# Optimization experiments

Measured on AMD Instinct MI355X. Metric: run time of the kernel, lower is better.

## Reference

```python
import jax, jax.numpy as jnp
import numpy as np

N, C, H, W = 16, 256, 64, 64
KC, VC, HEADS = 256, 256, 8

def setup_inputs() -> dict:
    key = jax.random.key(0)
    ks = jax.random.split(key, 9)
    s = 0.02
    return {
        "x": jax.random.normal(ks[0], (N, C, H, W), dtype=jnp.float32),
        "Wk": jax.random.normal(ks[1], (KC, C), dtype=jnp.float32) * s,
        "bk": jax.random.normal(ks[2], (KC,), dtype=jnp.float32) * s,
        "Wq": jax.random.normal(ks[3], (KC, C), dtype=jnp.float32) * s,
        "bq": jax.random.normal(ks[4], (KC,), dtype=jnp.float32) * s,
        "Wv": jax.random.normal(ks[5], (VC, C), dtype=jnp.float32) * s,
        "bv": jax.random.normal(ks[6], (VC,), dtype=jnp.float32) * s,
        "Wr": jax.random.normal(ks[7], (C, VC), dtype=jnp.float32) * s,
        "br": jax.random.normal(ks[8], (C,), dtype=jnp.float32) * s,
    }

def reference(x, Wk, bk, Wq, bq, Wv, bv, Wr, br):
    n, c, h, w = x.shape
    hw = h * w
    hk = KC // HEADS   # per-head key channels
    hv = VC // HEADS   # per-head value channels
    # 1x1 convs as channel matmuls
    keys = jnp.einsum('oi,nihw->nohw', Wk, x) + bk[None, :, None, None]
    queries = jnp.einsum('oi,nihw->nohw', Wq, x) + bq[None, :, None, None]
    values = jnp.einsum('oi,nihw->nohw', Wv, x) + bv[None, :, None, None]
    # split heads: (n, heads, ch_per_head, hw)
    k = keys.reshape(n, HEADS, hk, hw)
    q = queries.reshape(n, HEADS, hk, hw)
    v = values.reshape(n, HEADS, hv, hw)
    k = jax.nn.softmax(k, axis=3)   # softmax over spatial positions
    q = jax.nn.softmax(q, axis=2)   # softmax over key channels
    # context: (n, heads, hk, hv)
    ctx = jnp.einsum('nhkl,nhvl->nhkv', k, v)
    # attended: (n, heads, hv, hw)
    att = jnp.einsum('nhkv,nhkl->nhvl', ctx, q)
    agg = att.reshape(n, VC, h, w)
    out = jnp.einsum('ov,nvhw->nohw', Wr, agg) + br[None, :, None, None] + x
    return out
```

## Files before the change

### kernel.cpp

```cpp
#include <hip/hip_runtime.h>

#define NB   16
#define CD   256
#define HWD  4096

typedef __attribute__((ext_vector_type(8))) short short8;
typedef __attribute__((ext_vector_type(4))) float f32x4;

static __device__ __forceinline__ float b2f(unsigned short u) {
  union { unsigned int i; float f; } x; x.i = ((unsigned int)u) << 16; return x.f;
}
static __device__ __forceinline__ unsigned short f2b(float f) {
  union { float f; unsigned int i; } x; x.f = f;
  return (unsigned short)((x.i + 0x7fffu + ((x.i >> 16) & 1u)) >> 16);
}

static __device__ __forceinline__ void gload16(const void* g, const unsigned short* l) {
  __builtin_amdgcn_global_load_lds(
      (const __attribute__((address_space(1))) void*)g,
      (__attribute__((address_space(3))) void*)l, 16, 0, 0);
}

__global__ __launch_bounds__(256)
void prep_kernel(const float* __restrict__ Wk, const float* __restrict__ Wq,
                 const float* __restrict__ Wv, unsigned short* __restrict__ Wc)
{
  int e4 = blockIdx.x * 256 + threadIdx.x;
  int base = e4 * 4;
  int w = base >> 16, off = base & 65535;
  const float* W = (w == 0) ? Wk : (w == 1) ? Wq : Wv;
  f32x4 v = *(const f32x4*)(W + off);
  unsigned int lo = (unsigned int)f2b(v.x) | ((unsigned int)f2b(v.y) << 16);
  unsigned int hi = (unsigned int)f2b(v.z) | ((unsigned int)f2b(v.w) << 16);
  *(uint2*)(Wc + base) = make_uint2(lo, hi);
}

__global__ __launch_bounds__(256)
void xt_kernel(const float* __restrict__ x, unsigned short* __restrict__ xT)
{
  __shared__ __align__(16) unsigned short T[64 * 80];
  const int t = threadIdx.x;
  const int l0 = blockIdx.x * 64, c0 = blockIdx.y * 64, n = blockIdx.z;
  const float* xn = x + (size_t)n * CD * HWD;
#pragma unroll
  for (int i = 0; i < 4; ++i) {
    int idx = t + i * 256;
    int c = idx >> 4, l4 = (idx & 15) * 4;
    f32x4 v = *(const f32x4*)(xn + (size_t)(c0 + c) * HWD + l0 + l4);
    T[(l4 + 0) * 80 + c] = f2b(v.x);
    T[(l4 + 1) * 80 + c] = f2b(v.y);
    T[(l4 + 2) * 80 + c] = f2b(v.z);
    T[(l4 + 3) * 80 + c] = f2b(v.w);
  }
  __syncthreads();
  unsigned short* dst = xT + ((size_t)n * HWD + l0) * CD + c0;
#pragma unroll
  for (int i = 0; i < 2; ++i) {
    int e = t + i * 256;
    int lr = e >> 3, c8 = (e & 7) * 8;
    *(short8*)(dst + (size_t)lr * CD + c8) = *(const short8*)(T + lr * 80 + c8);
  }
}

__global__ __launch_bounds__(256, 4)
void kqv_kernel(const unsigned short* __restrict__ Wc,
                const unsigned short* __restrict__ xT,
                const float* __restrict__ bk, const float* __restrict__ bq,
                const float* __restrict__ bv,
                unsigned short* __restrict__ keys,
                unsigned short* __restrict__ qsmT,
                unsigned short* __restrict__ vals)
{
  __shared__ __align__(16) unsigned short smem[17408];

  const int t  = threadIdx.x;
  const int lt = blockIdx.x;
  const int mt = blockIdx.y;
  const int n  = blockIdx.z;
  const int l0 = lt * 128;
  const int m0 = mt * 128;
  const int wsel = m0 >> 8;
  const int ocbase = m0 & 255;

  const unsigned short* Ag  = Wc;
  const unsigned short* Btn = xT + (size_t)n * HWD * CD;

  const int w = t >> 6, lane = t & 63;
  const int wr = (w >> 1) * 64, wc = (w & 1) * 64;
  const int lhi = lane >> 4, llo = lane & 15;

  f32x4 acc[4][4] = {};

  auto stage = [&](int buf, int ks) {
    unsigned short* As = smem + buf * 8192;
    unsigned short* Bs = As + 4096;
    const int k0 = ks * 32;
#pragma unroll
    for (int i = 0; i < 2; ++i) {
      int s   = t + i * 256;
      int row = s >> 2;
      int src = (((s ^ row) & 3)) << 3;
      gload16(Ag  + (size_t)(m0 + row) * CD + k0 + src, As + s * 8);
      gload16(Btn + (size_t)(l0 + row) * CD + k0 + src, Bs + s * 8);
    }
  };

  auto compute = [&](int buf) {
    const unsigned short* As = smem + buf * 8192;
    const unsigned short* Bs = As + 4096;
    const int slot = (lhi ^ (llo & 3)) * 8;
    short8 a[4], b[4];
#pragma unroll
    for (int mi = 0; mi < 4; ++mi)
      a[mi] = *(const short8*)(As + (wr + mi * 16 + llo) * 32 + slot);
#pragma unroll
    for (int ni = 0; ni < 4; ++ni)
      b[ni] = *(const short8*)(Bs + (wc + ni * 16 + llo) * 32 + slot);
#pragma unroll
    for (int mi = 0; mi < 4; ++mi)
#pragma unroll
      for (int ni = 0; ni < 4; ++ni)
        acc[mi][ni] = __builtin_amdgcn_mfma_f32_16x16x32_bf16(a[mi], b[ni], acc[mi][ni], 0, 0, 0);
  };

  stage(0, 0);
  __syncthreads();
#pragma unroll
  for (int ks = 0; ks < 8; ++ks) {
    if (ks < 7) stage((ks + 1) & 1, ks + 1);
    compute(ks & 1);
    __syncthreads();
  }

  const float* bias = (wsel == 0) ? bk : (wsel == 1) ? bq : bv;
#pragma unroll
  for (int mi = 0; mi < 4; ++mi) {
#pragma unroll
    for (int r = 0; r < 4; ++r) {
      float bb = bias[ocbase + wr + mi * 16 + lhi * 4 + r];
#pragma unroll
      for (int ni = 0; ni < 4; ++ni) acc[mi][ni][r] += bb;
    }
  }

  if (wsel == 1) {
#pragma unroll
    for (int g = 0; g < 2; ++g) {
#pragma unroll
      for (int ni = 0; ni < 4; ++ni) {
        float m = -1e30f;
#pragma unroll
        for (int mi = 2 * g; mi < 2 * g + 2; ++mi)
#pragma unroll
          for (int r = 0; r < 4; ++r) m = fmaxf(m, acc[mi][ni][r]);
        m = fmaxf(m, __shfl_xor(m, 16));
        m = fmaxf(m, __shfl_xor(m, 32));
        float s = 0.f;
#pragma unroll
        for (int mi = 2 * g; mi < 2 * g + 2; ++mi)
#pragma unroll
          for (int r = 0; r < 4; ++r) {
            float e = __expf(acc[mi][ni][r] - m);
            acc[mi][ni][r] = e;
            s += e;
          }
        s += __shfl_xor(s, 16);
        s += __shfl_xor(s, 32);
        float inv = 1.f / s;
#pragma unroll
        for (int mi = 2 * g; mi < 2 * g + 2; ++mi)
#pragma unroll
          for (int r = 0; r < 4; ++r) acc[mi][ni][r] *= inv;
      }
    }
    unsigned short* Co2 = smem;
#pragma unroll
    for (int mi = 0; mi < 4; ++mi)
#pragma unroll
      for (int ni = 0; ni < 4; ++ni) {
        int col = wc + ni * 16 + llo;
#pragma unroll
        for (int r = 0; r < 4; ++r) {
          int row = wr + mi * 16 + lhi * 4 + r;
          Co2[col * 136 + row] = f2b(acc[mi][ni][r]);
        }
      }
    __syncthreads();
    unsigned short* dst = qsmT + ((size_t)n * HWD + l0) * CD + ocbase;
#pragma unroll
    for (int i = 0; i < 8; ++i) {
      int e = t + i * 256;
      int l = e >> 4, c8 = (e & 15) * 8;
      *(short8*)(dst + (size_t)l * CD + c8) = *(const short8*)(Co2 + l * 136 + c8);
    }
  } else {
    unsigned short* Co = smem;
#pragma unroll
    for (int mi = 0; mi < 4; ++mi)
#pragma unroll
      for (int ni = 0; ni < 4; ++ni) {
        int col = wc + ni * 16 + llo;
#pragma unroll
        for (int r = 0; r < 4; ++r) {
          int row = wr + mi * 16 + lhi * 4 + r;
          Co[row * 136 + col] = f2b(acc[mi][ni][r]);
        }
      }
    __syncthreads();
    unsigned short* dst = ((wsel == 0) ? keys : vals)
                          + ((size_t)(n * CD + (wsel == 0 ? ocbase : ocbase))) * HWD + l0;
#pragma unroll
    for (int i = 0; i < 8; ++i) {
      int e = t + i * 256;
      int row = e >> 4, c8 = (e & 15) * 8;
      *(short8*)(dst + (size_t)row * HWD + c8) = *(const short8*)(Co + row * 136 + c8);
    }
  }
}

__global__ __launch_bounds__(256)
void rowstats_kernel(const unsigned short* __restrict__ keys,
                     float* __restrict__ stats)
{
  __shared__ float red[8];
  const int r = blockIdx.x;
  const int t = threadIdx.x;
  const unsigned short* rowp = keys + (size_t)r * HWD;
  float v[16];
  float m = -1e30f;
#pragma unroll
  for (int i = 0; i < 2; ++i) {
    const short8 u = *(const short8*)(rowp + t * 8 + i * 2048);
#pragma unroll
    for (int j = 0; j < 8; ++j) {
      v[i * 8 + j] = b2f((unsigned short)u[j]);
      m = fmaxf(m, v[i * 8 + j]);
    }
  }
#pragma unroll
  for (int off = 1; off < 64; off <<= 1) m = fmaxf(m, __shfl_xor(m, off));
  if ((t & 63) == 0) red[t >> 6] = m;
  __syncthreads();
  m = fmaxf(fmaxf(red[0], red[1]), fmaxf(red[2], red[3]));
  float s = 0.f;
#pragma unroll
  for (int i = 0; i < 16; ++i) s += __expf(v[i] - m);
#pragma unroll
  for (int off = 1; off < 64; off <<= 1) s += __shfl_xor(s, off);
  if ((t & 63) == 0) red[4 + (t >> 6)] = s;
  __syncthreads();
  if (t == 0) {
    s = red[4] + red[5] + red[6] + red[7];
    stats[r * 2]     = m;
    stats[r * 2 + 1] = 1.f / s;
  }
}

__global__ __launch_bounds__(256)
void ctx_kernel(const unsigned short* __restrict__ keys,
                const unsigned short* __restrict__ vals,
                const float* __restrict__ stats,
                float* __restrict__ ctxp)
{
  __shared__ float Cs[4][32][33];
  const int hf = blockIdx.x;
  const int nh = blockIdx.y;
  const int n = nh >> 3, h = nh & 7;
  const int t = threadIdx.x, w = t >> 6, lane = t & 63;
  const int lhi = lane >> 4, llo = lane & 15;
  const int lbase = hf * 2048 + w * 512;

  const unsigned short* kr = keys + (size_t)(n * CD + h * 32) * HWD;
  const unsigned short* vr = vals + (size_t)(n * CD + h * 32) * HWD;

  float mx[2], inv[2];
#pragma unroll
  for (int mi = 0; mi < 2; ++mi) {
    int kc = mi * 16 + llo;
    mx[mi]  = stats[(n * CD + h * 32 + kc) * 2];
    inv[mi] = stats[(n * CD + h * 32 + kc) * 2 + 1];
  }

  f32x4 acc[2][2] = {};
  for (int ks = 0; ks < 16; ++ks) {
    const int loff = lbase + ks * 32 + lhi * 8;
    short8 a[2], b[2];
#pragma unroll
    for (int mi = 0; mi < 2; ++mi) {
      const short8 u = *(const short8*)(kr + (size_t)(mi * 16 + llo) * HWD + loff);
      short8 af;
#pragma unroll
      for (int j = 0; j < 8; ++j)
        af[j] = (short)f2b(__expf(b2f((unsigned short)u[j]) - mx[mi]) * inv[mi]);
      a[mi] = af;
    }
#pragma unroll
    for (int ni = 0; ni < 2; ++ni)
      b[ni] = *(const short8*)(vr + (size_t)(ni * 16 + llo) * HWD + loff);
    acc[0][0] = __builtin_amdgcn_mfma_f32_16x16x32_bf16(a[0], b[0], acc[0][0], 0, 0, 0);
    acc[0][1] = __builtin_amdgcn_mfma_f32_16x16x32_bf16(a[0], b[1], acc[0][1], 0, 0, 0);
    acc[1][0] = __builtin_amdgcn_mfma_f32_16x16x32_bf16(a[1], b[0], acc[1][0], 0, 0, 0);
    acc[1][1] = __builtin_amdgcn_mfma_f32_16x16x32_bf16(a[1], b[1], acc[1][1], 0, 0, 0);
  }

#pragma unroll
  for (int mi = 0; mi < 2; ++mi)
#pragma unroll
    for (int ni = 0; ni < 2; ++ni)
#pragma unroll
      for (int r = 0; r < 4; ++r)
        Cs[w][mi * 16 + lhi * 4 + r][ni * 16 + llo] = acc[mi][ni][r];
  __syncthreads();
#pragma unroll
  for (int i = 0; i < 4; ++i) {
    int e = t + i * 256;
    int kc = e >> 5, vc = e & 31;
    float sum = Cs[0][kc][vc] + Cs[1][kc][vc] + Cs[2][kc][vc] + Cs[3][kc][vc];
    ctxp[((size_t)hf * 128 + nh) * 1024 + e] = sum;
  }
}

__global__ __launch_bounds__(256)
void proj_kernel(const float* __restrict__ ctxp, const float* __restrict__ Wr,
                 unsigned short* __restrict__ M)
{
  __shared__ float cs[32][33];
  const int nh = blockIdx.x;
  const int n = nh >> 3, h = nh & 7;
  const int t = threadIdx.x;
#pragma unroll
  for (int i = 0; i < 4; ++i) {
    int e = t + i * 256;
    cs[e >> 5][e & 31] = ctxp[(size_t)nh * 1024 + e] + ctxp[((size_t)128 + nh) * 1024 + e];
  }
  __syncthreads();
  float wreg[32];
  const float* wp = Wr + (size_t)t * 256 + h * 32;
#pragma unroll
  for (int i = 0; i < 8; ++i) {
    f32x4 v = *(const f32x4*)(wp + i * 4);
    wreg[i * 4] = v.x; wreg[i * 4 + 1] = v.y; wreg[i * 4 + 2] = v.z; wreg[i * 4 + 3] = v.w;
  }
  unsigned short o16[32];
#pragma unroll
  for (int kc = 0; kc < 32; ++kc) {
    float s = 0.f;
#pragma unroll
    for (int vv = 0; vv < 32; ++vv) s += wreg[vv] * cs[kc][vv];
    o16[kc] = f2b(s);
  }
  unsigned short* mp = M + (size_t)(n * CD + t) * 256 + h * 32;
#pragma unroll
  for (int i = 0; i < 8; ++i) {
    unsigned int lo = (unsigned int)o16[i * 4]     | ((unsigned int)o16[i * 4 + 1] << 16);
    unsigned int hi = (unsigned int)o16[i * 4 + 2] | ((unsigned int)o16[i * 4 + 3] << 16);
    *(uint2*)(mp + i * 4) = make_uint2(lo, hi);
  }
}

__global__ __launch_bounds__(256, 4)
void out_kernel(const unsigned short* __restrict__ M,
                const unsigned short* __restrict__ qsmT,
                const float* __restrict__ br,
                const float* __restrict__ x,
                float* __restrict__ out)
{
  __shared__ __align__(16) unsigned short smem[16384];

  const int t = threadIdx.x;
  const int lt = blockIdx.x;
  const int mt = blockIdx.y;
  const int n  = blockIdx.z;
  const int l0 = lt * 128, m0 = mt * 128;

  const unsigned short* Ag  = M + (size_t)n * CD * 256;
  const unsigned short* Btn = qsmT + (size_t)n * HWD * CD;

  const int w = t >> 6, lane = t & 63;
  const int wr = (w >> 1) * 64, wc = (w & 1) * 64;
  const int lhi = lane >> 4, llo = lane & 15;

  f32x4 acc[4][4] = {};

  auto stage = [&](int buf, int ks) {
    unsigned short* As = smem + buf * 8192;
    unsigned short* Bs = As + 4096;
    const int k0 = ks * 32;
#pragma unroll
    for (int i = 0; i < 2; ++i) {
      int s   = t + i * 256;
      int row = s >> 2;
      int src = (((s ^ row) & 3)) << 3;
      gload16(Ag  + (size_t)(m0 + row) * CD + k0 + src, As + s * 8);
      gload16(Btn + (size_t)(l0 + row) * CD + k0 + src, Bs + s * 8);
    }
  };

  auto compute = [&](int buf) {
    const unsigned short* As = smem + buf * 8192;
    const unsigned short* Bs = As + 4096;
    const int slot = (lhi ^ (llo & 3)) * 8;
    short8 a[4], b[4];
#pragma unroll
    for (int mi = 0; mi < 4; ++mi)
      a[mi] = *(const short8*)(As + (wr + mi * 16 + llo) * 32 + slot);
#pragma unroll
    for (int ni = 0; ni < 4; ++ni)
      b[ni] = *(const short8*)(Bs + (wc + ni * 16 + llo) * 32 + slot);
#pragma unroll
    for (int mi = 0; mi < 4; ++mi)
#pragma unroll
      for (int ni = 0; ni < 4; ++ni)
        acc[mi][ni] = __builtin_amdgcn_mfma_f32_16x16x32_bf16(a[mi], b[ni], acc[mi][ni], 0, 0, 0);
  };

  stage(0, 0);
  __syncthreads();
#pragma unroll
  for (int ks = 0; ks < 8; ++ks) {
    if (ks < 7) stage((ks + 1) & 1, ks + 1);
    compute(ks & 1);
    __syncthreads();
  }

  const float* xn = x + (size_t)n * CD * HWD;
  float* on = out + (size_t)n * CD * HWD;
#pragma unroll
  for (int mi = 0; mi < 4; ++mi)
#pragma unroll
    for (int r = 0; r < 4; ++r) {
      int row = m0 + wr + mi * 16 + lhi * 4 + r;
      float bb = br[row];
#pragma unroll
      for (int ni = 0; ni < 4; ++ni) {
        int col = l0 + wc + ni * 16 + llo;
        size_t off = (size_t)row * HWD + col;
        on[off] = acc[mi][ni][r] + bb + xn[off];
      }
    }
}

extern "C" void kernel_launch(void* const* d_in, const int* in_sizes, int n_in,
                              void* d_out, int out_size, void* d_ws, size_t ws_size,
                              hipStream_t stream) {
  const float* x  = (const float*)d_in[0];
  const float* Wk = (const float*)d_in[1];
  const float* bk = (const float*)d_in[2];
  const float* Wq = (const float*)d_in[3];
  const float* bq = (const float*)d_in[4];
  const float* Wv = (const float*)d_in[5];
  const float* bv = (const float*)d_in[6];
  const float* Wr = (const float*)d_in[7];
  const float* br = (const float*)d_in[8];
  float* out = (float*)d_out;

  char* ws = (char*)d_ws;
  unsigned short* keys = (unsigned short*)(ws);
  unsigned short* vals = (unsigned short*)(ws + 33554432);
  unsigned short* qsmT = (unsigned short*)(ws + 67108864);
  float* stats         = (float*)(ws + 100663296);
  float* ctxp          = (float*)(ws + 100696064);
  unsigned short* M    = (unsigned short*)(ws + 101744640);
  unsigned short* Wc   = (unsigned short*)(ws + 103841792);
  unsigned short* xT   = (unsigned short*)d_out;

  hipLaunchKernelGGL(prep_kernel, dim3(192), dim3(256), 0, stream, Wk, Wq, Wv, Wc);
  hipLaunchKernelGGL(xt_kernel, dim3(64, 4, NB), dim3(256), 0, stream, x, xT);
  hipLaunchKernelGGL(kqv_kernel, dim3(32, 6, NB), dim3(256), 0, stream,
                     Wc, xT, bk, bq, bv, keys, qsmT, vals);
  hipLaunchKernelGGL(rowstats_kernel, dim3(NB * CD), dim3(256), 0, stream, keys, stats);
  hipLaunchKernelGGL(ctx_kernel, dim3(2, 128), dim3(256), 0, stream,
                     keys, vals, stats, ctxp);
  hipLaunchKernelGGL(proj_kernel, dim3(128), dim3(256), 0, stream, ctxp, Wr, M);
  hipLaunchKernelGGL(out_kernel, dim3(32, 2, NB), dim3(256), 0, stream,
                     M, qsmT, br, x, out);
}
```

Measured before the change: 144.2 us.

## Use 64x64 output tiles with full-K single-shot LDS staging in out_kernel

The output GEMM kernel moves from 128x128 tiles with a double-buffered K loop of 32-wide stages to 64x64 tiles that load the entire K=256 slab of both operands into LDS at once, with a new XOR swizzle. The grid grows fourfold (64x4x16 blocks) and each wave computes a 2x2 MFMA block. The aim is more parallelism and fewer barriers in the memory-bound epilogue that reads x and writes out. The cost is lower data reuse per tile, more redundant loads of M and qsmT, and 64KB of LDS per block, which reduces occupancy (launch bounds drop to 2).

```diff
diff --git a/kernel.cpp b/kernel.cpp
--- a/kernel.cpp
+++ b/kernel.cpp
@@ -208,7 +208,7 @@
       }
     __syncthreads();
     unsigned short* dst = ((wsel == 0) ? keys : vals)
-                          + ((size_t)(n * CD + (wsel == 0 ? ocbase : ocbase))) * HWD + l0;
+                          + ((size_t)(n * CD + ocbase)) * HWD + l0;
 #pragma unroll
     for (int i = 0; i < 8; ++i) {
       int e = t + i * 256;
@@ -358,81 +358,74 @@
   }
 }
 
-__global__ __launch_bounds__(256, 4)
+__global__ __launch_bounds__(256, 2)
 void out_kernel(const unsigned short* __restrict__ M,
                 const unsigned short* __restrict__ qsmT,
                 const float* __restrict__ br,
                 const float* __restrict__ x,
                 float* __restrict__ out)
 {
-  __shared__ __align__(16) unsigned short smem[16384];
-
-  const int t = threadIdx.x;
+  __shared__ __align__(16) unsigned short smem[32768];
+  unsigned short* As = smem;
+  unsigned short* Bs = smem + 16384;
+
+  const int t  = threadIdx.x;
   const int lt = blockIdx.x;
   const int mt = blockIdx.y;
   const int n  = blockIdx.z;
-  const int l0 = lt * 128, m0 = mt * 128;
+  const int l0 = lt * 64, m0 = mt * 64;
 
   const unsigned short* Ag  = M + (size_t)n * CD * 256;
   const unsigned short* Btn = qsmT + (size_t)n * HWD * CD;
 
-  const int w = t >> 6, lane = t & 63;
-  const int wr = (w >> 1) * 64, wc = (w & 1) * 64;
+  const int wid = t >> 6, lane = t & 63;
+  const int wr = (wid >> 1) * 32, wc = (wid & 1) * 32;
   const int lhi = lane >> 4, llo = lane & 15;
 
-  f32x4 acc[4][4] = {};
-
-  auto stage = [&](int buf, int ks) {
-    unsigned short* As = smem + buf * 8192;
-    unsigned short* Bs = As + 4096;
-    const int k0 = ks * 32;
-#pragma unroll
-    for (int i = 0; i < 2; ++i) {
-      int s   = t + i * 256;
-      int row = s >> 2;
-      int src = (((s ^ row) & 3)) << 3;
-      gload16(Ag  + (size_t)(m0 + row) * CD + k0 + src, As + s * 8);
-      gload16(Btn + (size_t)(l0 + row) * CD + k0 + src, Bs + s * 8);
-    }
-  };
-
-  auto compute = [&](int buf) {
-    const unsigned short* As = smem + buf * 8192;
-    const unsigned short* Bs = As + 4096;
-    const int slot = (lhi ^ (llo & 3)) * 8;
-    short8 a[4], b[4];
-#pragma unroll
-    for (int mi = 0; mi < 4; ++mi)
-      a[mi] = *(const short8*)(As + (wr + mi * 16 + llo) * 32 + slot);
-#pragma unroll
-    for (int ni = 0; ni < 4; ++ni)
-      b[ni] = *(const short8*)(Bs + (wc + ni * 16 + llo) * 32 + slot);
-#pragma unroll
-    for (int mi = 0; mi < 4; ++mi)
-#pragma unroll
-      for (int ni = 0; ni < 4; ++ni)
+#pragma unroll
+  for (int i = 0; i < 8; ++i) {
+    int s = t + i * 256;
+    int R = s >> 5, sl = s & 31;
+    int srcsl = (sl & 24) | ((sl ^ R) & 7);
+    gload16(Ag  + (size_t)(m0 + R) * CD + srcsl * 8, As + s * 8);
+    gload16(Btn + (size_t)(l0 + R) * CD + srcsl * 8, Bs + s * 8);
+  }
+  __syncthreads();
+
+  f32x4 acc[2][2] = {};
+#pragma unroll
+  for (int ks = 0; ks < 8; ++ks) {
+    int jg = ks * 4 + lhi;
+    short8 a[2], b[2];
+#pragma unroll
+    for (int mi = 0; mi < 2; ++mi) {
+      int R = wr + mi * 16 + llo;
+      int pj = (jg & 24) | ((jg ^ (R & 7)) & 7);
+      a[mi] = *(const short8*)(As + R * 256 + pj * 8);
+    }
+#pragma unroll
+    for (int ni = 0; ni < 2; ++ni) {
+      int l = wc + ni * 16 + llo;
+      int pj = (jg & 24) | ((jg ^ (l & 7)) & 7);
+      b[ni] = *(const short8*)(Bs + l * 256 + pj * 8);
+    }
+#pragma unroll
+    for (int mi = 0; mi < 2; ++mi)
+#pragma unroll
+      for (int ni = 0; ni < 2; ++ni)
         acc[mi][ni] = __builtin_amdgcn_mfma_f32_16x16x32_bf16(a[mi], b[ni], acc[mi][ni], 0, 0, 0);
-  };
-
-  stage(0, 0);
-  __syncthreads();
-#pragma unroll
-  for (int ks = 0; ks < 8; ++ks) {
-    if (ks < 7) stage((ks + 1) & 1, ks + 1);
-    compute(ks & 1);
-    __syncthreads();
   }
 
   const float* xn = x + (size_t)n * CD * HWD;
   float* on = out + (size_t)n * CD * HWD;
 #pragma unroll
-  for (int mi = 0; mi < 4; ++mi)
+  for (int mi = 0; mi < 2; ++mi)
 #pragma unroll
     for (int r = 0; r < 4; ++r) {
       int row = m0 + wr + mi * 16 + lhi * 4 + r;
       float bb = br[row];
 #pragma unroll
-      for (int ni = 0; ni < 4; ++ni) {
+      for (int ni = 0; ni < 2; ++ni) {
         int col = l0 + wc + ni * 16 + llo;
         size_t off = (size_t)row * HWD + col;
         on[off] = acc[mi][ni][r] + bb + xn[off];
@@ -472,6 +465,6 @@
   hipLaunchKernelGGL(ctx_kernel, dim3(2, 128), dim3(256), 0, stream,
                      keys, vals, stats, ctxp);
   hipLaunchKernelGGL(proj_kernel, dim3(128), dim3(256), 0, stream, ctxp, Wr, M);
-  hipLaunchKernelGGL(out_kernel, dim3(32, 2, NB), dim3(256), 0, stream,
+  hipLaunchKernelGGL(out_kernel, dim3(64, 4, NB), dim3(256), 0, stream,
                      M, qsmT, br, x, out);
 }
```

Result: faster. 133.6 us (-7.3%).
